# Kernel optimization log

Hardware: AMD Instinct MI355X
Metric: run time of the kernel (lower is better)

Reference implementation:

```python
import jax, jax.numpy as jnp
import numpy as np

N_WIN = 7      # region grid (BiFormer default)
NUM_HEADS = 8
TOPK = 4
EPS = 1e-5

def layernorm(x, g, b):
    mu = x.mean(-1, keepdims=True)
    var = ((x - mu) ** 2).mean(-1, keepdims=True)
    return (x - mu) * jax.lax.rsqrt(var + EPS) * g + b

def bilevel_routing_attn(x, wqkv, bqkv, wo, bo):
    B, H, W, C = x.shape
    h, w = H // N_WIN, W // N_WIN          # region size (8,8)
    R, r = N_WIN * N_WIN, h * w            # 49 regions, 64 tokens each
    d = C // NUM_HEADS
    scale = 1.0 / jnp.sqrt(jnp.asarray(d, x.dtype))
    qkv = x @ wqkv + bqkv                  # (B,H,W,3C)
    q, k, v = jnp.split(qkv, 3, axis=-1)
    def to_regions(t):
        t = t.reshape(B, N_WIN, h, N_WIN, w, C).transpose(0, 1, 3, 2, 4, 5)
        return t.reshape(B, R, r, C)
    qr, kr, vr = to_regions(q), to_regions(k), to_regions(v)
    # coarse region-level routing
    q_reg = qr.mean(2)                     # (B,R,C)
    k_reg = kr.mean(2)
    logits = jnp.einsum('brc,bsc->brs', q_reg, k_reg)   # (B,R,R)
    _, idx = jax.lax.top_k(logits, TOPK)   # (B,R,TOPK)
    # gather top-k regions' k/v: out[b,i,j] = kr[b, idx[b,i,j]]
    idx_e = idx[:, :, :, None, None]       # (B,R,TOPK,1,1)
    kg = jnp.take_along_axis(kr[:, None], idx_e, axis=2).reshape(B, R, TOPK * r, C)
    vg = jnp.take_along_axis(vr[:, None], idx_e, axis=2).reshape(B, R, TOPK * r, C)
    # fine-grained multi-head attention within routed regions
    qh = qr.reshape(B, R, r, NUM_HEADS, d)
    kh = kg.reshape(B, R, TOPK * r, NUM_HEADS, d)
    vh = vg.reshape(B, R, TOPK * r, NUM_HEADS, d)
    scores = jnp.einsum('brqhd,brkhd->brhqk', qh, kh) * scale
    attn = jax.nn.softmax(scores, axis=-1)
    out = jnp.einsum('brhqk,brkhd->brqhd', attn, vh).reshape(B, R, r, C)
    # regions back to image layout
    out = out.reshape(B, N_WIN, N_WIN, h, w, C).transpose(0, 1, 3, 2, 4, 5)
    out = out.reshape(B, H, W, C)
    return out @ wo + bo

def mlp(x, w1, bm1, w2, bm2):
    return jax.nn.gelu(x @ w1 + bm1) @ w2 + bm2

def setup_inputs() -> dict:
    key = jax.random.key(0)
    ks = jax.random.split(key, 5)
    C = 256
    s = lambda fan: 1.0 / np.sqrt(fan)
    return {
        'x': jax.random.normal(ks[0], (8, 56, 56, C), jnp.float32),
        'ln1_g': jnp.ones((C,), jnp.float32),
        'ln1_b': jnp.zeros((C,), jnp.float32),
        'wqkv': jax.random.normal(ks[1], (C, 3 * C), jnp.float32) * s(C),
        'bqkv': jnp.zeros((3 * C,), jnp.float32),
        'wo': jax.random.normal(ks[2], (C, C), jnp.float32) * s(C),
        'bo': jnp.zeros((C,), jnp.float32),
        'ln2_g': jnp.ones((C,), jnp.float32),
        'ln2_b': jnp.zeros((C,), jnp.float32),
        'w1': jax.random.normal(ks[3], (C, 4 * C), jnp.float32) * s(C),
        'bm1': jnp.zeros((4 * C,), jnp.float32),
        'w2': jax.random.normal(ks[4], (4 * C, C), jnp.float32) * s(4 * C),
        'bm2': jnp.zeros((C,), jnp.float32),
    }

def reference(x, ln1_g, ln1_b, wqkv, bqkv, wo, bo, ln2_g, ln2_b, w1, bm1, w2, bm2):
    x = x + bilevel_routing_attn(layernorm(x, ln1_g, ln1_b), wqkv, bqkv, wo, bo)
    x = x + mlp(layernorm(x, ln2_g, ln2_b), w1, bm1, w2, bm2)
    return x
```

## Files before the change

kernel.cpp:

```cpp
#include <hip/hip_runtime.h>
#include <math.h>

#define CDIM 256
#define QKVDIM 768
#define NHEADS 8
#define DHEAD 32
#define NWIN 7
#define NREG 49
#define TK 4
static constexpr int NROWS = 8 * 56 * 56;

typedef __attribute__((ext_vector_type(8))) short s16x8;
typedef __attribute__((ext_vector_type(4))) float f32x4;
typedef __attribute__((ext_vector_type(16))) float f32x16;
typedef unsigned short ushort_t;

union U4 { unsigned u[4]; s16x8 v; };

__device__ __forceinline__ ushort_t bfr(float f) {
    unsigned u = __float_as_uint(f);
    unsigned r = (u + 0x7FFFu + ((u >> 16) & 1u)) >> 16;
    return (ushort_t)r;
}
__device__ __forceinline__ float gelu_f(float x) {
    float u = 0.7978845608028654f * (x + 0.044715f * x * x * x);
    return 0.5f * x * (1.0f + tanhf(u));
}
__device__ __forceinline__ void glds16(const void* g, void* l) {
    __builtin_amdgcn_global_load_lds((const __attribute__((address_space(1))) void*)g,
                                     (__attribute__((address_space(3))) void*)l, 16, 0, 0);
}
__device__ __forceinline__ f32x16 zero16() {
    f32x16 z;
#pragma unroll
    for (int i = 0; i < 16; i++) z[i] = 0.f;
    return z;
}

__global__ __launch_bounds__(256) void ln_kernel(const float* __restrict__ x,
                                                 const float* __restrict__ g,
                                                 const float* __restrict__ bparam,
                                                 ushort_t* __restrict__ y) {
    int wave = threadIdx.x >> 6, lane = threadIdx.x & 63;
    int row = blockIdx.x * 4 + wave;
    const float4* xr = (const float4*)(x + (size_t)row * CDIM);
    float4 v = xr[lane];
    float s = v.x + v.y + v.z + v.w;
    float s2 = v.x * v.x + v.y * v.y + v.z * v.z + v.w * v.w;
#pragma unroll
    for (int off = 32; off; off >>= 1) {
        s += __shfl_xor(s, off, 64);
        s2 += __shfl_xor(s2, off, 64);
    }
    float mu = s * (1.0f / CDIM);
    float rstd = rsqrtf(s2 * (1.0f / CDIM) - mu * mu + 1e-5f);
    float4 gv = ((const float4*)g)[lane];
    float4 bv = ((const float4*)bparam)[lane];
    ushort4 o;
    o.x = bfr((v.x - mu) * rstd * gv.x + bv.x);
    o.y = bfr((v.y - mu) * rstd * gv.y + bv.y);
    o.z = bfr((v.z - mu) * rstd * gv.z + bv.z);
    o.w = bfr((v.w - mu) * rstd * gv.w + bv.w);
    *(ushort4*)(y + (size_t)row * CDIM + lane * 4) = o;
}

__global__ __launch_bounds__(256) void ymean_kernel(const float* __restrict__ x,
                                                    const float* __restrict__ g,
                                                    const float* __restrict__ bparam,
                                                    float* __restrict__ ymean) {
    int blk = blockIdx.x;
    int b = blk / NREG, rid = blk % NREG;
    int ai = rid / NWIN, aj = rid % NWIN;
    int w = threadIdx.x >> 6, lane = threadIdx.x & 63;
    float4 gv = ((const float4*)g)[lane];
    float4 bv = ((const float4*)bparam)[lane];
    float4 acc = {0.f, 0.f, 0.f, 0.f};
    for (int it = 0; it < 16; it++) {
        int t = it * 4 + w;
        size_t row = ((size_t)(b * 56 + ai * 8 + (t >> 3))) * 56 + aj * 8 + (t & 7);
        float4 v = ((const float4*)(x + row * CDIM))[lane];
        float s = v.x + v.y + v.z + v.w;
        float s2 = v.x * v.x + v.y * v.y + v.z * v.z + v.w * v.w;
#pragma unroll
        for (int off = 32; off; off >>= 1) {
            s += __shfl_xor(s, off, 64);
            s2 += __shfl_xor(s2, off, 64);
        }
        float mu = s * (1.0f / CDIM);
        float rstd = rsqrtf(s2 * (1.0f / CDIM) - mu * mu + 1e-5f);
        acc.x += (v.x - mu) * rstd * gv.x + bv.x;
        acc.y += (v.y - mu) * rstd * gv.y + bv.y;
        acc.z += (v.z - mu) * rstd * gv.z + bv.z;
        acc.w += (v.w - mu) * rstd * gv.w + bv.w;
    }
    __shared__ float red[4][CDIM];
    *(float4*)&red[w][lane * 4] = acc;
    __syncthreads();
    if (w == 0) {
        float4 r0 = *(float4*)&red[0][lane * 4];
        float4 r1 = *(float4*)&red[1][lane * 4];
        float4 r2 = *(float4*)&red[2][lane * 4];
        float4 r3 = *(float4*)&red[3][lane * 4];
        float4 o;
        o.x = (r0.x + r1.x + r2.x + r3.x) * (1.0f / 64.0f);
        o.y = (r0.y + r1.y + r2.y + r3.y) * (1.0f / 64.0f);
        o.z = (r0.z + r1.z + r2.z + r3.z) * (1.0f / 64.0f);
        o.w = (r0.w + r1.w + r2.w + r3.w) * (1.0f / 64.0f);
        *(float4*)(ymean + (size_t)blk * CDIM + lane * 4) = o;
    }
}

__global__ __launch_bounds__(256) void regproj_kernel(const float* __restrict__ ymean,
                                                      const float* __restrict__ wqkv,
                                                      const float* __restrict__ bqkv,
                                                      float* __restrict__ qreg,
                                                      float* __restrict__ kreg) {
    int blk = blockIdx.x;
    __shared__ float ym[CDIM];
    ym[threadIdx.x] = ymean[(size_t)blk * CDIM + threadIdx.x];
    __syncthreads();
    int c = threadIdx.x;
    float sq = 0.f, sk = 0.f;
    for (int k = 0; k < CDIM; k++) {
        float yv = ym[k];
        sq = fmaf(yv, wqkv[(size_t)k * QKVDIM + c], sq);
        sk = fmaf(yv, wqkv[(size_t)k * QKVDIM + CDIM + c], sk);
    }
    qreg[(size_t)blk * CDIM + c] = sq + bqkv[c];
    kreg[(size_t)blk * CDIM + c] = sk + bqkv[CDIM + c];
}

__global__ __launch_bounds__(256) void wtrans_kernel(const float* __restrict__ src,
                                                     ushort_t* __restrict__ dst,
                                                     int K, int N) {
    __shared__ float t[32][33];
    int tx = threadIdx.x & 31, ty = threadIdx.x >> 5;
    int n0 = blockIdx.x * 32, k0 = blockIdx.y * 32;
#pragma unroll
    for (int i = 0; i < 4; i++) t[ty + i * 8][tx] = src[(size_t)(k0 + ty + i * 8) * N + n0 + tx];
    __syncthreads();
#pragma unroll
    for (int i = 0; i < 4; i++)
        dst[(size_t)(n0 + ty + i * 8) * K + k0 + tx] = bfr(t[tx][ty + i * 8]);
}

__global__ __launch_bounds__(256) void vtrans_kernel(const ushort_t* __restrict__ qkvbf,
                                                     ushort_t* __restrict__ vt) {
    __shared__ ushort_t t[32][34];
    int tx = threadIdx.x & 31, ty = threadIdx.x >> 5;
    int t0 = blockIdx.x * 32, c0 = blockIdx.y * 32, b = blockIdx.z;
#pragma unroll
    for (int i = 0; i < 4; i++)
        t[ty + i * 8][tx] = qkvbf[((size_t)b * 3136 + t0 + ty + i * 8) * QKVDIM + 512 + c0 + tx];
    __syncthreads();
#pragma unroll
    for (int i = 0; i < 4; i++)
        vt[((size_t)b * CDIM + c0 + ty + i * 8) * 3136 + t0 + tx] = t[tx][ty + i * 8];
}

template <int MODE>
__global__ __launch_bounds__(256) void mgemm(const ushort_t* __restrict__ A,
                                             const ushort_t* __restrict__ WT,
                                             const float* __restrict__ bias,
                                             const float* __restrict__ res,
                                             float* __restrict__ outf,
                                             ushort_t* __restrict__ outb,
                                             int N, int K) {
    __shared__ __align__(16) ushort_t As[128 * 64];
    __shared__ __align__(16) ushort_t Bs[128 * 64];
    const int tid = threadIdx.x, lane = tid & 63, w = tid >> 6;
    const int wm = w >> 1, wn = w & 1;
    const int tm = blockIdx.y * 128, tn = blockIdx.x * 128;
    f32x4 acc[4][4];
#pragma unroll
    for (int i = 0; i < 4; i++)
#pragma unroll
        for (int j = 0; j < 4; j++) acc[i][j] = (f32x4){0.f, 0.f, 0.f, 0.f};

    for (int k0 = 0; k0 < K; k0 += 64) {
        __syncthreads();
#pragma unroll
        for (int p = 0; p < 4; p++) {
            int row = (p * 4 + w) * 8 + (lane >> 3);
            int slot = lane & 7;
            glds16(A + (size_t)(tm + row) * K + k0 + ((slot ^ (row & 7)) * 8),
                   (char*)As + (p * 4 + w) * 1024);
            glds16(WT + (size_t)(tn + row) * K + k0 + ((slot ^ (row & 7)) * 8),
                   (char*)Bs + (p * 4 + w) * 1024);
        }
        __syncthreads();
#pragma unroll
        for (int kk = 0; kk < 2; kk++) {
            s16x8 af[4], bfv[4];
#pragma unroll
            for (int i = 0; i < 4; i++) {
                int rowa = wm * 64 + i * 16 + (lane & 15);
                af[i] = *(const s16x8*)&As[rowa * 64 + (((kk * 4 + (lane >> 4)) ^ (rowa & 7)) * 8)];
                int rowb = wn * 64 + i * 16 + (lane & 15);
                bfv[i] = *(const s16x8*)&Bs[rowb * 64 + (((kk * 4 + (lane >> 4)) ^ (rowb & 7)) * 8)];
            }
#pragma unroll
            for (int i = 0; i < 4; i++)
#pragma unroll
                for (int j = 0; j < 4; j++)
                    acc[i][j] = __builtin_amdgcn_mfma_f32_16x16x32_bf16(af[i], bfv[j], acc[i][j], 0, 0, 0);
        }
    }
    const int cl = lane & 15, gq = lane >> 4;
#pragma unroll
    for (int j = 0; j < 4; j++) {
        int col = tn + wn * 64 + j * 16 + cl;
        float bb = bias[col];
#pragma unroll
        for (int i = 0; i < 4; i++) {
            int rowb = tm + wm * 64 + i * 16 + gq * 4;
#pragma unroll
            for (int r = 0; r < 4; r++) {
                float v = acc[i][j][r] + bb;
                size_t off = (size_t)(rowb + r) * N + col;
                if (MODE == 0) {
                    outb[off] = bfr(col < 256 ? v * 0.17677669529663687f : v);
                } else if (MODE == 1 || MODE == 3) {
                    outf[off] = v + res[off];
                } else {
                    outb[off] = bfr(gelu_f(v));
                }
            }
        }
    }
}

__global__ __launch_bounds__(64) void routing_kernel(const float* __restrict__ qreg,
                                                     const float* __restrict__ kreg,
                                                     int* __restrict__ idx) {
    int b = blockIdx.x / NREG;
    int row = blockIdx.x % NREG;
    int lane = threadIdx.x;
    float myv = -INFINITY;
    if (lane < NREG) {
        const float* qv = qreg + ((size_t)b * NREG + row) * CDIM;
        const float* kv = kreg + ((size_t)b * NREG + lane) * CDIM;
        float s = 0.f;
        for (int c = 0; c < CDIM; c++) s += qv[c] * kv[c];
        myv = s;
    }
    for (int t = 0; t < TK; t++) {
        float v = myv;
        int ix = lane;
#pragma unroll
        for (int off = 32; off; off >>= 1) {
            float ov = __shfl_xor(v, off, 64);
            int oi = __shfl_xor(ix, off, 64);
            if (ov > v || (ov == v && oi < ix)) { v = ov; ix = oi; }
        }
        if (lane == 0) idx[((size_t)b * NREG + row) * TK + t] = ix;
        if (lane == ix) myv = -INFINITY;
    }
}

__global__ __launch_bounds__(256) void attn2_kernel(const ushort_t* __restrict__ qk,
                                                    const ushort_t* __restrict__ vt,
                                                    const int* __restrict__ idx,
                                                    ushort_t* __restrict__ outb) {
    int wid = blockIdx.x * 4 + (threadIdx.x >> 6);
    int lane = threadIdx.x & 63;
    int g = lane >> 5, col = lane & 31;
    int qh = wid & 1;
    int h = (wid >> 1) & 7;
    int rr = wid >> 4;
    int rid = rr % NREG, b = rr / NREG;
    int ai = rid / NWIN, aj = rid % NWIN;

    int qtok = qh * 32 + col;
    size_t qrow_g = ((size_t)(b * 56 + ai * 8 + (qtok >> 3))) * 56 + aj * 8 + (qtok & 7);
    const s16x8 bq0 = *(const s16x8*)(qk + qrow_g * QKVDIM + h * 32 + g * 8);
    const s16x8 bq1 = *(const s16x8*)(qk + qrow_g * QKVDIM + h * 32 + 16 + g * 8);

    const int* ip = idx + (size_t)rr * TK;
    int regs[4] = {ip[0], ip[1], ip[2], ip[3]};

    float m_run = -1e30f, l_run = 0.f;
    f32x16 o = zero16();
    const size_t vtrowbase = ((size_t)(b * CDIM + h * 32 + col)) * 3136;

#pragma unroll
    for (int rc = 0; rc < 4; rc++) {
        int reg = regs[rc];
        int rai = reg / NWIN, raj = reg % NWIN;
        s16x8 ka[2][2];
#pragma unroll
        for (int mf = 0; mf < 2; mf++) {
            int ktok = mf * 32 + col;
            size_t krow_g = ((size_t)(b * 56 + rai * 8 + (ktok >> 3))) * 56 + raj * 8 + (ktok & 7);
#pragma unroll
            for (int kd = 0; kd < 2; kd++)
                ka[mf][kd] = *(const s16x8*)(qk + krow_g * QKVDIM + 256 + h * 32 + kd * 16 + g * 8);
        }
        f32x16 s0 = zero16(), s1 = zero16();
        s0 = __builtin_amdgcn_mfma_f32_32x32x16_bf16(ka[0][0], bq0, s0, 0, 0, 0);
        s0 = __builtin_amdgcn_mfma_f32_32x32x16_bf16(ka[0][1], bq1, s0, 0, 0, 0);
        s1 = __builtin_amdgcn_mfma_f32_32x32x16_bf16(ka[1][0], bq0, s1, 0, 0, 0);
        s1 = __builtin_amdgcn_mfma_f32_32x32x16_bf16(ka[1][1], bq1, s1, 0, 0, 0);

        float tmax = -1e30f;
#pragma unroll
        for (int i = 0; i < 16; i++) tmax = fmaxf(tmax, fmaxf(s0[i], s1[i]));
        tmax = fmaxf(tmax, __shfl_xor(tmax, 32, 64));

        float m_new = fmaxf(m_run, tmax);
        float f = __expf(m_run - m_new);
        l_run *= f;
#pragma unroll
        for (int r = 0; r < 16; r++) {
            int orow = (r & 3) + 8 * (r >> 2) + 4 * g;
            float fr = __shfl(f, orow, 64);
            o[r] *= fr;
        }
        m_run = m_new;

        float tsum = 0.f;
#pragma unroll
        for (int i = 0; i < 16; i++) {
            s0[i] = __expf(s0[i] - m_run);
            s1[i] = __expf(s1[i] - m_run);
            tsum += s0[i] + s1[i];
        }
        l_run += tsum + __shfl_xor(tsum, 32, 64);

#define PVSTEP(SS, CC, KS)                                                              \
    {                                                                                   \
        unsigned wa = (unsigned)bfr(SS[CC * 8 + 0]) | ((unsigned)bfr(SS[CC * 8 + 1]) << 16); \
        unsigned wb_ = (unsigned)bfr(SS[CC * 8 + 2]) | ((unsigned)bfr(SS[CC * 8 + 3]) << 16); \
        unsigned wc = (unsigned)bfr(SS[CC * 8 + 4]) | ((unsigned)bfr(SS[CC * 8 + 5]) << 16); \
        unsigned wd = (unsigned)bfr(SS[CC * 8 + 6]) | ((unsigned)bfr(SS[CC * 8 + 7]) << 16); \
        unsigned sxa = (unsigned)__shfl_xor((int)wa, 32, 64);                           \
        unsigned sxb = (unsigned)__shfl_xor((int)wb_, 32, 64);                          \
        unsigned sxc = (unsigned)__shfl_xor((int)wc, 32, 64);                           \
        unsigned sxd = (unsigned)__shfl_xor((int)wd, 32, 64);                           \
        U4 pw;                                                                          \
        pw.u[0] = g ? sxc : wa;                                                         \
        pw.u[1] = g ? sxd : wb_;                                                        \
        pw.u[2] = g ? wc : sxa;                                                         \
        pw.u[3] = g ? wd : sxb;                                                         \
        const s16x8 vb = *(const s16x8*)(vt + vtrowbase + (size_t)(rai * 8 + KS * 2 + g) * 56 + raj * 8); \
        o = __builtin_amdgcn_mfma_f32_32x32x16_bf16(pw.v, vb, o, 0, 0, 0);              \
    }
        PVSTEP(s0, 0, 0)
        PVSTEP(s0, 1, 1)
        PVSTEP(s1, 0, 2)
        PVSTEP(s1, 1, 3)
#undef PVSTEP
    }

#pragma unroll
    for (int r = 0; r < 16; r++) {
        int orow = (r & 3) + 8 * (r >> 2) + 4 * g;
        float lr = __shfl(l_run, orow, 64);
        float val = o[r] / lr;
        int tok = qh * 32 + orow;
        size_t row_g = ((size_t)(b * 56 + ai * 8 + (tok >> 3))) * 56 + aj * 8 + (tok & 7);
        outb[row_g * 256 + h * 32 + col] = bfr(val);
    }
}

extern "C" void kernel_launch(void* const* d_in, const int* in_sizes, int n_in,
                              void* d_out, int out_size, void* d_ws, size_t ws_size,
                              hipStream_t stream) {
    const float* x    = (const float*)d_in[0];
    const float* ln1g = (const float*)d_in[1];
    const float* ln1b = (const float*)d_in[2];
    const float* wqkv = (const float*)d_in[3];
    const float* bqkv = (const float*)d_in[4];
    const float* wo   = (const float*)d_in[5];
    const float* bo   = (const float*)d_in[6];
    const float* ln2g = (const float*)d_in[7];
    const float* ln2b = (const float*)d_in[8];
    const float* w1   = (const float*)d_in[9];
    const float* bm1  = (const float*)d_in[10];
    const float* w2   = (const float*)d_in[11];
    const float* bm2  = (const float*)d_in[12];
    float* out = (float*)d_out;
    char* ws = (char*)d_ws;

    ushort_t* ws_qkvbf = (ushort_t*)(ws);
    ushort_t* ws_hbf   = (ushort_t*)(ws + 38535168);
    ushort_t* ws_ybf   = (ushort_t*)(ws + 89915392);
    ushort_t* ws_vt    = (ushort_t*)(ws + 102760448);
    ushort_t* ws_attn  = (ushort_t*)(ws + 115605504);
    float*    ws_ymean = (float*)(ws + 128450560);
    float*    ws_qreg  = (float*)(ws + 128851968);
    float*    ws_kreg  = (float*)(ws + 129253376);
    int*      ws_idx   = (int*)(ws + 129654784);
    ushort_t* ws_wqkvT = (ushort_t*)(ws + 129661056);
    ushort_t* ws_woT   = (ushort_t*)(ws + 130054272);
    ushort_t* ws_w1T   = (ushort_t*)(ws + 130185344);
    ushort_t* ws_w2T   = (ushort_t*)(ws + 130709632);

    const int M = NROWS;

    wtrans_kernel<<<dim3(768 / 32, 256 / 32), 256, 0, stream>>>(wqkv, ws_wqkvT, 256, 768);
    wtrans_kernel<<<dim3(256 / 32, 256 / 32), 256, 0, stream>>>(wo, ws_woT, 256, 256);
    wtrans_kernel<<<dim3(1024 / 32, 256 / 32), 256, 0, stream>>>(w1, ws_w1T, 256, 1024);
    wtrans_kernel<<<dim3(256 / 32, 1024 / 32), 256, 0, stream>>>(w2, ws_w2T, 1024, 256);
    ln_kernel<<<M / 4, 256, 0, stream>>>(x, ln1g, ln1b, ws_ybf);
    ymean_kernel<<<8 * NREG, 256, 0, stream>>>(x, ln1g, ln1b, ws_ymean);
    regproj_kernel<<<8 * NREG, 256, 0, stream>>>(ws_ymean, wqkv, bqkv, ws_qreg, ws_kreg);
    routing_kernel<<<8 * NREG, 64, 0, stream>>>(ws_qreg, ws_kreg, ws_idx);
    mgemm<0><<<dim3(QKVDIM / 128, M / 128), 256, 0, stream>>>(
        ws_ybf, ws_wqkvT, bqkv, nullptr, nullptr, ws_qkvbf, QKVDIM, CDIM);
    vtrans_kernel<<<dim3(3136 / 32, 256 / 32, 8), 256, 0, stream>>>(ws_qkvbf, ws_vt);
    attn2_kernel<<<8 * NREG * NHEADS * 2 / 4, 256, 0, stream>>>(ws_qkvbf, ws_vt, ws_idx, ws_attn);
    mgemm<1><<<dim3(CDIM / 128, M / 128), 256, 0, stream>>>(
        ws_attn, ws_woT, bo, x, out, nullptr, CDIM, CDIM);
    ln_kernel<<<M / 4, 256, 0, stream>>>(out, ln2g, ln2b, ws_ybf);
    mgemm<2><<<dim3(1024 / 128, M / 128), 256, 0, stream>>>(
        ws_ybf, ws_w1T, bm1, nullptr, nullptr, ws_hbf, 1024, CDIM);
    mgemm<3><<<dim3(CDIM / 128, M / 128), 256, 0, stream>>>(
        ws_hbf, ws_w2T, bm2, out, out, nullptr, CDIM, 1024);
}
```

Measured before the change: 333.2 us.

## Double-buffer GEMM K-loop with async LDS prefetch, block swizzle, narrower N tiles

```diff
diff --git a/kernel.cpp b/kernel.cpp
--- a/kernel.cpp
+++ b/kernel.cpp
@@ -29,6 +29,15 @@
 __device__ __forceinline__ void glds16(const void* g, void* l) {
     __builtin_amdgcn_global_load_lds((const __attribute__((address_space(1))) void*)g,
                                      (__attribute__((address_space(3))) void*)l, 16, 0, 0);
+}
+template <int N>
+__device__ __forceinline__ void waitvm() {
+    if constexpr (N == 0) asm volatile("s_waitcnt vmcnt(0)" ::: "memory");
+    else if constexpr (N == 3) asm volatile("s_waitcnt vmcnt(3)" ::: "memory");
+    else if constexpr (N == 4) asm volatile("s_waitcnt vmcnt(4)" ::: "memory");
+}
+__device__ __forceinline__ void barrier_raw() {
+    asm volatile("s_barrier" ::: "memory");
 }
 __device__ __forceinline__ f32x16 zero16() {
     f32x16 z;
@@ -158,7 +167,7 @@
         vt[((size_t)b * CDIM + c0 + ty + i * 8) * 3136 + t0 + tx] = t[tx][ty + i * 8];
 }
 
-template <int MODE>
+template <int BM, int BN, int MODE>
 __global__ __launch_bounds__(256) void mgemm(const ushort_t* __restrict__ A,
                                              const ushort_t* __restrict__ WT,
                                              const float* __restrict__ bias,
@@ -166,54 +175,85 @@
                                              float* __restrict__ outf,
                                              ushort_t* __restrict__ outb,
                                              int N, int K) {
-    __shared__ __align__(16) ushort_t As[128 * 64];
-    __shared__ __align__(16) ushort_t Bs[128 * 64];
+    constexpr int WM = BM / 2, WN = BN / 2, MI = WM / 16, NI = WN / 16;
+    constexpr int RA = BM / 64, RB = BN / 64, L = RA + RB;
+    __shared__ __align__(16) ushort_t As[2 * BM * 32];
+    __shared__ __align__(16) ushort_t Bs[2 * BN * 32];
     const int tid = threadIdx.x, lane = tid & 63, w = tid >> 6;
     const int wm = w >> 1, wn = w & 1;
-    const int tm = blockIdx.y * 128, tn = blockIdx.x * 128;
-    f32x4 acc[4][4];
-#pragma unroll
-    for (int i = 0; i < 4; i++)
-#pragma unroll
-        for (int j = 0; j < 4; j++) acc[i][j] = (f32x4){0.f, 0.f, 0.f, 0.f};
-
-    for (int k0 = 0; k0 < K; k0 += 64) {
-        __syncthreads();
-#pragma unroll
-        for (int p = 0; p < 4; p++) {
-            int row = (p * 4 + w) * 8 + (lane >> 3);
-            int slot = lane & 7;
-            glds16(A + (size_t)(tm + row) * K + k0 + ((slot ^ (row & 7)) * 8),
-                   (char*)As + (p * 4 + w) * 1024);
-            glds16(WT + (size_t)(tn + row) * K + k0 + ((slot ^ (row & 7)) * 8),
-                   (char*)Bs + (p * 4 + w) * 1024);
-        }
-        __syncthreads();
-#pragma unroll
-        for (int kk = 0; kk < 2; kk++) {
-            s16x8 af[4], bfv[4];
-#pragma unroll
-            for (int i = 0; i < 4; i++) {
-                int rowa = wm * 64 + i * 16 + (lane & 15);
-                af[i] = *(const s16x8*)&As[rowa * 64 + (((kk * 4 + (lane >> 4)) ^ (rowa & 7)) * 8)];
-                int rowb = wn * 64 + i * 16 + (lane & 15);
-                bfv[i] = *(const s16x8*)&Bs[rowb * 64 + (((kk * 4 + (lane >> 4)) ^ (rowb & 7)) * 8)];
-            }
-#pragma unroll
-            for (int i = 0; i < 4; i++)
-#pragma unroll
-                for (int j = 0; j < 4; j++)
-                    acc[i][j] = __builtin_amdgcn_mfma_f32_16x16x32_bf16(af[i], bfv[j], acc[i][j], 0, 0, 0);
-        }
-    }
+
+    const int gx = gridDim.x;
+    const int nwg = gx * gridDim.y;
+    const int bid = blockIdx.y * gx + blockIdx.x;
+    const int lbid = (bid & 7) * (nwg >> 3) + (bid >> 3);
+    const int tm = (lbid / gx) * BM, tn = (lbid % gx) * BN;
+
+    f32x4 acc[MI][NI];
+#pragma unroll
+    for (int i = 0; i < MI; i++)
+#pragma unroll
+        for (int j = 0; j < NI; j++) acc[i][j] = (f32x4){0.f, 0.f, 0.f, 0.f};
+
+    auto stage = [&](int buf, int k0) {
+#pragma unroll
+        for (int p = 0; p < RA; p++) {
+            int row = (p * 4 + w) * 16 + (lane >> 2);
+            int slot = lane & 3;
+            int mr = (row ^ (row >> 2)) & 3;
+            glds16(A + (size_t)(tm + row) * K + k0 + ((slot ^ mr) * 8),
+                   (char*)As + buf * BM * 64 + (p * 4 + w) * 1024);
+        }
+#pragma unroll
+        for (int p = 0; p < RB; p++) {
+            int row = (p * 4 + w) * 16 + (lane >> 2);
+            int slot = lane & 3;
+            int mr = (row ^ (row >> 2)) & 3;
+            glds16(WT + (size_t)(tn + row) * K + k0 + ((slot ^ mr) * 8),
+                   (char*)Bs + buf * BN * 64 + (p * 4 + w) * 1024);
+        }
+    };
+
+    const int NT = K >> 5;
+    const int fr = lane & 15, sl = lane >> 4;
+    stage(0, 0);
+    for (int kt = 0; kt < NT; ++kt) {
+        int cur = kt & 1;
+        if (kt + 1 < NT) {
+            stage(cur ^ 1, (kt + 1) * 32);
+            waitvm<L>();
+        } else {
+            waitvm<0>();
+        }
+        barrier_raw();
+        s16x8 af[MI], bfv[NI];
+#pragma unroll
+        for (int i = 0; i < MI; i++) {
+            int rowa = wm * WM + i * 16 + fr;
+            int ma = (rowa ^ (rowa >> 2)) & 3;
+            af[i] = *(const s16x8*)&As[cur * BM * 32 + rowa * 32 + ((sl ^ ma) * 8)];
+        }
+#pragma unroll
+        for (int j = 0; j < NI; j++) {
+            int rowb = wn * WN + j * 16 + fr;
+            int mb = (rowb ^ (rowb >> 2)) & 3;
+            bfv[j] = *(const s16x8*)&Bs[cur * BN * 32 + rowb * 32 + ((sl ^ mb) * 8)];
+        }
+#pragma unroll
+        for (int i = 0; i < MI; i++)
+#pragma unroll
+            for (int j = 0; j < NI; j++)
+                acc[i][j] = __builtin_amdgcn_mfma_f32_16x16x32_bf16(af[i], bfv[j], acc[i][j], 0, 0, 0);
+        barrier_raw();
+    }
+
     const int cl = lane & 15, gq = lane >> 4;
 #pragma unroll
-    for (int j = 0; j < 4; j++) {
-        int col = tn + wn * 64 + j * 16 + cl;
+    for (int j = 0; j < NI; j++) {
+        int col = tn + wn * WN + j * 16 + cl;
         float bb = bias[col];
 #pragma unroll
-        for (int i = 0; i < 4; i++) {
-            int rowb = tm + wm * 64 + i * 16 + gq * 4;
+        for (int i = 0; i < MI; i++) {
+            int rowb = tm + wm * WM + i * 16 + gq * 4;
 #pragma unroll
             for (int r = 0; r < 4; r++) {
                 float v = acc[i][j][r] + bb;
@@ -406,15 +446,15 @@
     ymean_kernel<<<8 * NREG, 256, 0, stream>>>(x, ln1g, ln1b, ws_ymean);
     regproj_kernel<<<8 * NREG, 256, 0, stream>>>(ws_ymean, wqkv, bqkv, ws_qreg, ws_kreg);
     routing_kernel<<<8 * NREG, 64, 0, stream>>>(ws_qreg, ws_kreg, ws_idx);
-    mgemm<0><<<dim3(QKVDIM / 128, M / 128), 256, 0, stream>>>(
+    mgemm<128, 128, 0><<<dim3(QKVDIM / 128, M / 128), 256, 0, stream>>>(
         ws_ybf, ws_wqkvT, bqkv, nullptr, nullptr, ws_qkvbf, QKVDIM, CDIM);
     vtrans_kernel<<<dim3(3136 / 32, 256 / 32, 8), 256, 0, stream>>>(ws_qkvbf, ws_vt);
     attn2_kernel<<<8 * NREG * NHEADS * 2 / 4, 256, 0, stream>>>(ws_qkvbf, ws_vt, ws_idx, ws_attn);
-    mgemm<1><<<dim3(CDIM / 128, M / 128), 256, 0, stream>>>(
+    mgemm<128, 64, 1><<<dim3(CDIM / 64, M / 128), 256, 0, stream>>>(
         ws_attn, ws_woT, bo, x, out, nullptr, CDIM, CDIM);
     ln_kernel<<<M / 4, 256, 0, stream>>>(out, ln2g, ln2b, ws_ybf);
-    mgemm<2><<<dim3(1024 / 128, M / 128), 256, 0, stream>>>(
+    mgemm<128, 128, 2><<<dim3(1024 / 128, M / 128), 256, 0, stream>>>(
         ws_ybf, ws_w1T, bm1, nullptr, nullptr, ws_hbf, 1024, CDIM);
-    mgemm<3><<<dim3(CDIM / 128, M / 128), 256, 0, stream>>>(
+    mgemm<128, 64, 3><<<dim3(CDIM / 64, M / 128), 256, 0, stream>>>(
         ws_hbf, ws_w2T, bm2, out, out, nullptr, CDIM, 1024);
 }
```

Result: faster. 321.4 us (-3.5%).
